# Performance work log

Measured on AMD Instinct MI355X. Metric: run time of the kernel, lower is better.

The kernel has to match this reference:

```python
import jax, jax.numpy as jnp
import numpy as np

# Static config matching AdaConv(c_in=512, p=4, batch_size=8, s_d=512, c_out=512)
C_IN = 512
C_OUT = 512
N_GROUPS = 128  # c_in // p


def _conv(x, w, b, groups=1, padding='VALID'):
    # x: NCHW, w: OIHW
    y = jax.lax.conv_general_dilated(
        x, w, window_strides=(1, 1), padding=padding,
        dimension_numbers=('NCHW', 'OIHW', 'NCHW'),
        feature_group_count=groups)
    return y + b[None, :, None, None]


def setup_inputs() -> dict:
    key = jax.random.key(0)
    ks = jax.random.split(key, 9)
    f32 = jnp.float32
    s = 0.02  # small init scale to keep activations well-behaved
    inp = {
        'style_encoding': jax.random.normal(ks[0], (8, 512, 4, 4), f32),
        'predicted': jax.random.normal(ks[1], (8, 512, 64, 64), f32),
        'dw1_w': jax.random.normal(ks[2], (512, 512, 1, 1), f32) * s,
        'dw1_b': jnp.full((512,), 0.01, f32),
        'dw2_w': jax.random.normal(ks[3], (2048, 512, 2, 2), f32) * s,
        'dw2_b': jnp.full((2048,), 0.01, f32),
        'pk1_w': jax.random.normal(ks[4], (512, 512, 1, 1), f32) * s,
        'pk1_b': jnp.full((512,), 0.01, f32),
        'pk2_w': jax.random.normal(ks[5], (2048, 512, 1, 1), f32) * s,
        'pk2_b': jnp.full((2048,), 0.01, f32),
        'pb1_w': jax.random.normal(ks[6], (512, 512, 1, 1), f32) * s,
        'pb1_b': jnp.full((512,), 0.01, f32),
        'pb2_w': jax.random.normal(ks[7], (512, 512, 1, 1), f32) * s,
        'pb2_b': jnp.full((512,), 0.01, f32),
    }
    return inp


def reference(style_encoding, predicted,
              dw1_w, dw1_b, dw2_w, dw2_b,
              pk1_w, pk1_b, pk2_w, pk2_b,
              pb1_w, pb1_b, pb2_w, pb2_b):
    N = style_encoding.shape[0]
    lrelu = lambda x: jax.nn.leaky_relu(x, 0.01)

    # --- predict per-sample depthwise 3x3 kernels from style (4x4 -> 3x3) ---
    h = lrelu(_conv(style_encoding, dw1_w, dw1_b))           # [N, c_in, 4, 4]
    depthwise = _conv(h, dw2_w, dw2_b)                       # [N, c_out*(c_in/n_groups), 3, 3]
    depthwise = depthwise.reshape(N * C_OUT, C_IN // N_GROUPS, 3, 3)

    # --- predict per-sample pointwise kernels + bias from pooled style ---
    s_pool = jnp.mean(style_encoding, axis=(2, 3), keepdims=True)  # [N, s_d, 1, 1]
    pk = _conv(lrelu(_conv(s_pool, pk1_w, pk1_b)), pk2_w, pk2_b)
    pointwise_kn = pk.reshape(N * C_OUT, C_OUT // N_GROUPS, 1, 1)
    pb = _conv(lrelu(_conv(s_pool, pb1_w, pb1_b)), pb2_w, pb2_b)
    pointwise_bias = pb.reshape(N * C_OUT)

    # --- apply per-sample dynamic conv via huge-group grouped conv trick ---
    a, b, c, d = predicted.shape
    x = predicted.reshape(1, a * b, c, d)
    x = jnp.pad(x, ((0, 0), (0, 0), (1, 1), (1, 1)), mode='reflect')
    batch_groups = N * N_GROUPS
    y = jax.lax.conv_general_dilated(
        x, depthwise, (1, 1), 'VALID',
        dimension_numbers=('NCHW', 'OIHW', 'NCHW'),
        feature_group_count=batch_groups)                    # [1, N*c_out, c, d]
    y = jax.lax.conv_general_dilated(
        y, pointwise_kn, (1, 1), 'VALID',
        dimension_numbers=('NCHW', 'OIHW', 'NCHW'),
        feature_group_count=batch_groups)
    y = y + pointwise_bias[None, :, None, None]
    # permute([1,0,2,3]).view(a,b,c,d) with leading dim 1 == plain reshape
    return y.reshape(a, b, c, d)
```

## Files before the change

### kernel.cpp

```cpp
#include <hip/hip_runtime.h>

#define LRELU(x) ((x) > 0.f ? (x) : 0.01f * (x))

#define H2_OFF    0
#define T1_OFF    65536
#define T2_OFF    69632
#define PK_OFF    73728
#define PB_OFF    90112
#define D_OFF     94208
#define WB_OFF    241664

__global__ __launch_bounds__(256) void kA(const float* __restrict__ style,
    const float* __restrict__ dw1_w, const float* __restrict__ dw1_b,
    const float* __restrict__ pk1_w, const float* __restrict__ pk1_b,
    const float* __restrict__ pb1_w, const float* __restrict__ pb1_b,
    float* __restrict__ h2, float* __restrict__ t1, float* __restrict__ t2,
    float* __restrict__ D) {
  int b = blockIdx.x;
  int tid = threadIdx.x;
  __shared__ float smem[512];
  if (b >= 576) {
    int idx = (b - 576) * 256 + tid;
    float4 z; z.x = 0.f; z.y = 0.f; z.z = 0.f; z.w = 0.f;
    for (int j = idx; j < 36864; j += 16384) ((float4*)D)[j] = z;
    return;
  }
  int wave = tid >> 6, l = tid & 63;
  float sv[8];
  const float* w;
  const float* bv;
  float* outp;
  int cobase;
  bool relu;
  if (b < 512) {
    int n = b >> 6; int pix = (b >> 2) & 15; int cq = b & 3;
    const float* sp = style + n * 8192 + pix;
#pragma unroll
    for (int j = 0; j < 8; ++j) sv[j] = sp[(8 * l + j) * 16];
    w = dw1_w; bv = dw1_b;
    cobase = cq * 128 + wave * 32;
    outp = h2 + n * 8192 + pix * 512;
    relu = true;
  } else {
    int b2 = b - 512;
    int cq = b2 & 3; int which = (b2 >> 2) & 1; int n = b2 >> 3;
    for (int ci = tid; ci < 512; ci += 256) {
      const float4* r4 = (const float4*)(style + n * 8192 + ci * 16);
      float4 a = r4[0], bb = r4[1], c = r4[2], d = r4[3];
      smem[ci] = (a.x+a.y+a.z+a.w + bb.x+bb.y+bb.z+bb.w + c.x+c.y+c.z+c.w + d.x+d.y+d.z+d.w) * (1.f/16.f);
    }
    __syncthreads();
#pragma unroll
    for (int j = 0; j < 8; ++j) sv[j] = smem[8 * l + j];
    w  = which ? pb1_w : pk1_w;
    bv = which ? pb1_b : pk1_b;
    cobase = cq * 128 + wave * 32;
    outp = (which ? t2 : t1) + n * 512;
    relu = true;
  }
  float res = (l < 32) ? bv[cobase + l] : 0.f;
#pragma unroll 8
  for (int j = 0; j < 32; ++j) {
    int co = cobase + j;
    const float4* wr = (const float4*)(w + co * 512 + 8 * l);
    float4 a = wr[0], c = wr[1];
    float v = a.x*sv[0] + a.y*sv[1] + a.z*sv[2] + a.w*sv[3]
            + c.x*sv[4] + c.y*sv[5] + c.z*sv[6] + c.w*sv[7];
    v += __shfl_xor(v, 1);
    v += __shfl_xor(v, 2);
    v += __shfl_xor(v, 4);
    v += __shfl_xor(v, 8);
    v += __shfl_xor(v, 16);
    v += __shfl_xor(v, 32);
    if (l == j) res += v;
  }
  if (l < 32) {
    float o = relu ? LRELU(res) : res;
    outp[cobase + l] = o;
  }
}

__global__ __launch_bounds__(256) void kB(const float* __restrict__ h2,
    const float* __restrict__ dw2_w,
    const float* __restrict__ t1, const float* __restrict__ t2,
    const float* __restrict__ pk2_w, const float* __restrict__ pk2_b,
    const float* __restrict__ pb2_w, const float* __restrict__ pb2_b,
    float* __restrict__ D, float* __restrict__ pk, float* __restrict__ pb) {
  __shared__ float smem[1280];
  int b = blockIdx.x;
  int tid = threadIdx.x;
  if (b < 512) {
    int kc = b & 31; int bt = b >> 5; int bo = bt & 7; int nh = bt >> 3;
    {
      int pix = tid & 15; int ci4 = (tid >> 4) & 3; int nn = tid >> 6;
      const float* src = h2 + (nh * 4 + nn) * 8192 + pix * 512 + kc * 16 + ci4 * 4;
      float4 v = *(const float4*)src;
      float* dst = &smem[(nn * 16 + ci4 * 4) * 20 + pix];
      dst[0]  = v.x;
      dst[20] = v.y;
      dst[40] = v.z;
      dst[60] = v.w;
    }
    __syncthreads();
    int o2 = bo * 256 + tid;
    const float4* wr = (const float4*)(dw2_w + o2 * 2048 + kc * 64);
    float acc[4][9];
#pragma unroll
    for (int nn = 0; nn < 4; ++nn)
#pragma unroll
      for (int p = 0; p < 9; ++p) acc[nn][p] = 0.f;
    for (int ci = 0; ci < 16; ++ci) {
      float4 wv = wr[ci];
#pragma unroll
      for (int nn = 0; nn < 4; ++nn) {
        const float* hrow = &smem[(nn * 16 + ci) * 20];
        float4 a0 = *(const float4*)(hrow + 0);
        float4 a1 = *(const float4*)(hrow + 4);
        float4 a2 = *(const float4*)(hrow + 8);
        float4 a3 = *(const float4*)(hrow + 12);
        float vv[16];
        vv[0]=a0.x; vv[1]=a0.y; vv[2]=a0.z; vv[3]=a0.w;
        vv[4]=a1.x; vv[5]=a1.y; vv[6]=a1.z; vv[7]=a1.w;
        vv[8]=a2.x; vv[9]=a2.y; vv[10]=a2.z; vv[11]=a2.w;
        vv[12]=a3.x; vv[13]=a3.y; vv[14]=a3.z; vv[15]=a3.w;
#pragma unroll
        for (int p = 0; p < 9; ++p) {
          int r = (p / 3) * 4 + (p % 3);
          acc[nn][p] += wv.x * vv[r] + wv.y * vv[r + 1] + wv.z * vv[r + 4] + wv.w * vv[r + 5];
        }
      }
    }
#pragma unroll
    for (int nn = 0; nn < 4; ++nn)
#pragma unroll
      for (int p = 0; p < 9; ++p)
        atomicAdd(&D[((nh * 4 + nn) * 9 + p) * 2048 + o2], acc[nn][p]);
  } else {
    int idx = b - 512;
    int n = idx / 10; int tile = idx % 10;
    bool isPb = tile >= 8;
    float* s = smem;
    const float* src = (isPb ? t2 : t1) + n * 512;
    for (int i = tid; i < 512; i += 256) s[i] = src[i];
    __syncthreads();
    int o = (isPb ? tile - 8 : tile) * 256 + tid;
    const float* w = isPb ? pb2_w : pk2_w;
    float acc = (isPb ? pb2_b : pk2_b)[o];
    const float4* wr = (const float4*)(w + o * 512);
#pragma unroll 8
    for (int k = 0; k < 128; ++k) {
      float4 wv = wr[k];
      acc += wv.x * s[4*k] + wv.y * s[4*k+1] + wv.z * s[4*k+2] + wv.w * s[4*k+3];
    }
    if (isPb) pb[n * 512 + o] = acc; else pk[n * 2048 + o] = acc;
  }
}

__global__ __launch_bounds__(256) void kW(const float* __restrict__ D,
    const float* __restrict__ pk, const float* __restrict__ dw2_b,
    const float* __restrict__ pb, float* __restrict__ wbuf) {
  int idx = blockIdx.x * 256 + threadIdx.x;
  if (idx >= 8 * 128 * 160) return;
  int t = idx % 160; int Qn = idx / 160; int Q = Qn & 127; int n = Qn >> 7;
  if (t >= 144) {
    wbuf[idx] = (t < 148) ? pb[n * 512 + Q * 4 + (t - 144)] : 0.f;
    return;
  }
  int o = t & 3; int u = t >> 2; int kx = u % 3; int v = u / 3;
  int i = v & 3; int ky = v >> 2; int p = ky * 3 + kx;
  const float* Dp  = D + (n * 9 + p) * 2048 + 16 * Q;
  const float* pkp = pk + n * 2048 + 16 * Q + 4 * o;
  const float* bp  = dw2_b + 16 * Q;
  float sum = 0.f;
#pragma unroll
  for (int j = 0; j < 4; ++j) sum += pkp[j] * (Dp[4 * j + i] + bp[4 * j + i]);
  wbuf[idx] = sum;
}

__global__ __launch_bounds__(256) void kC(const float* __restrict__ x,
    const float* __restrict__ wbuf, float* __restrict__ out) {
  int b = blockIdx.x; int rt = b & 3; int Q = (b >> 2) & 127; int n = b >> 9;
  const float* wb = wbuf + (size_t)(n * 128 + Q) * 160;
  const float* base = x + (size_t)(n * 512 + Q * 4) * 4096;
  int e = threadIdx.x & 15;
  int y = rt * 16 + (threadIdx.x >> 4);
  int x0 = 4 * e;
  int ro[3];
#pragma unroll
  for (int ky = 0; ky < 3; ++ky) {
    int ry = y - 1 + ky;
    ry = ry < 0 ? 1 : (ry > 63 ? 62 : ry);
    ro[ky] = ry * 64;
  }
  float acc[4][4];
#pragma unroll
  for (int o = 0; o < 4; ++o) {
    float bv = wb[144 + o];
#pragma unroll
    for (int px = 0; px < 4; ++px) acc[o][px] = bv;
  }
#pragma unroll
  for (int i = 0; i < 4; ++i) {
    const float* ci = base + i * 4096;
#pragma unroll
    for (int ky = 0; ky < 3; ++ky) {
      float4 v0 = *(const float4*)(ci + ro[ky] + x0);
      float vl = __shfl_up(v0.w, 1, 16);
      float vr = __shfl_down(v0.x, 1, 16);
      if (e == 0)  vl = v0.y;
      if (e == 15) vr = v0.z;
      float va0 = vl, va1 = v0.x, va2 = v0.y, va3 = v0.z, va4 = v0.w, va5 = vr;
#pragma unroll
      for (int kx = 0; kx < 3; ++kx) {
        const float* wp = &wb[((ky * 4 + i) * 3 + kx) * 4];
        float w0 = wp[0], w1 = wp[1], w2 = wp[2], w3 = wp[3];
        float xv0 = kx == 0 ? va0 : (kx == 1 ? va1 : va2);
        float xv1 = kx == 0 ? va1 : (kx == 1 ? va2 : va3);
        float xv2 = kx == 0 ? va2 : (kx == 1 ? va3 : va4);
        float xv3 = kx == 0 ? va3 : (kx == 1 ? va4 : va5);
        acc[0][0] += w0 * xv0; acc[0][1] += w0 * xv1; acc[0][2] += w0 * xv2; acc[0][3] += w0 * xv3;
        acc[1][0] += w1 * xv0; acc[1][1] += w1 * xv1; acc[1][2] += w1 * xv2; acc[1][3] += w1 * xv3;
        acc[2][0] += w2 * xv0; acc[2][1] += w2 * xv1; acc[2][2] += w2 * xv2; acc[2][3] += w2 * xv3;
        acc[3][0] += w3 * xv0; acc[3][1] += w3 * xv1; acc[3][2] += w3 * xv2; acc[3][3] += w3 * xv3;
      }
    }
  }
#pragma unroll
  for (int o = 0; o < 4; ++o) {
    float4 st; st.x = acc[o][0]; st.y = acc[o][1]; st.z = acc[o][2]; st.w = acc[o][3];
    *(float4*)&out[(((size_t)(n * 512 + Q * 4 + o)) * 64 + y) * 64 + x0] = st;
  }
}

extern "C" void kernel_launch(void* const* d_in, const int* in_sizes, int n_in,
                              void* d_out, int out_size, void* d_ws, size_t ws_size,
                              hipStream_t stream) {
  const float* style = (const float*)d_in[0];
  const float* pred  = (const float*)d_in[1];
  const float* dw1_w = (const float*)d_in[2];
  const float* dw1_b = (const float*)d_in[3];
  const float* dw2_w = (const float*)d_in[4];
  const float* dw2_b = (const float*)d_in[5];
  const float* pk1_w = (const float*)d_in[6];
  const float* pk1_b = (const float*)d_in[7];
  const float* pk2_w = (const float*)d_in[8];
  const float* pk2_b = (const float*)d_in[9];
  const float* pb1_w = (const float*)d_in[10];
  const float* pb1_b = (const float*)d_in[11];
  const float* pb2_w = (const float*)d_in[12];
  const float* pb2_b = (const float*)d_in[13];
  float* ws = (float*)d_ws;
  float* h2 = ws + H2_OFF;
  float* t1 = ws + T1_OFF;
  float* t2 = ws + T2_OFF;
  float* pk = ws + PK_OFF;
  float* pb = ws + PB_OFF;
  float* D  = ws + D_OFF;
  float* wb = ws + WB_OFF;
  float* out = (float*)d_out;

  kA<<<640, 256, 0, stream>>>(style, dw1_w, dw1_b, pk1_w, pk1_b, pb1_w, pb1_b, h2, t1, t2, D);
  kB<<<592, 256, 0, stream>>>(h2, dw2_w, t1, t2, pk2_w, pk2_b, pb2_w, pb2_b, D, pk, pb);
  kW<<<640, 256, 0, stream>>>(D, pk, dw2_b, pb, wb);
  kC<<<4096, 256, 0, stream>>>(pred, wb, out);
}
```

Measured before the change: 86.67 us.

## Stage dw2 weights through LDS with coalesced loads and split kB finer

The dw2 part of kB now loads its weight tile cooperatively into shared memory with coalesced float4 reads, replacing per-thread strided row reads. The input-channel chunk is halved, so there are twice as many blocks and twice as many atomicAdds into D. The pk2/pb2 matvec is rewritten to use the wave-wide shuffle-reduction pattern, which gives coalesced weight rows instead of one row per thread. LDS use rises to about 39KB per block, which may lower occupancy.

```diff
diff --git a/kernel.cpp b/kernel.cpp
--- a/kernel.cpp
+++ b/kernel.cpp
@@ -31,7 +31,6 @@
   const float* bv;
   float* outp;
   int cobase;
-  bool relu;
   if (b < 512) {
     int n = b >> 6; int pix = (b >> 2) & 15; int cq = b & 3;
     const float* sp = style + n * 8192 + pix;
@@ -40,7 +39,6 @@
     w = dw1_w; bv = dw1_b;
     cobase = cq * 128 + wave * 32;
     outp = h2 + n * 8192 + pix * 512;
-    relu = true;
   } else {
     int b2 = b - 512;
     int cq = b2 & 3; int which = (b2 >> 2) & 1; int n = b2 >> 3;
@@ -56,7 +54,6 @@
     bv = which ? pb1_b : pk1_b;
     cobase = cq * 128 + wave * 32;
     outp = (which ? t2 : t1) + n * 512;
-    relu = true;
   }
   float res = (l < 32) ? bv[cobase + l] : 0.f;
 #pragma unroll 8
@@ -74,10 +71,7 @@
     v += __shfl_xor(v, 32);
     if (l == j) res += v;
   }
-  if (l < 32) {
-    float o = relu ? LRELU(res) : res;
-    outp[cobase + l] = o;
-  }
+  if (l < 32) outp[cobase + l] = LRELU(res);
 }
 
 __global__ __launch_bounds__(256) void kB(const float* __restrict__ h2,
@@ -86,34 +80,43 @@
     const float* __restrict__ pk2_w, const float* __restrict__ pk2_b,
     const float* __restrict__ pb2_w, const float* __restrict__ pb2_b,
     float* __restrict__ D, float* __restrict__ pk, float* __restrict__ pb) {
-  __shared__ float smem[1280];
+  __shared__ float smem[9856];
   int b = blockIdx.x;
   int tid = threadIdx.x;
-  if (b < 512) {
-    int kc = b & 31; int bt = b >> 5; int bo = bt & 7; int nh = bt >> 3;
-    {
-      int pix = tid & 15; int ci4 = (tid >> 4) & 3; int nn = tid >> 6;
-      const float* src = h2 + (nh * 4 + nn) * 8192 + pix * 512 + kc * 16 + ci4 * 4;
+  if (b < 1024) {
+    int kc = b & 63; int bo = (b >> 6) & 7; int nh = b >> 9;
+    float* Wt = smem;
+    float* ht = smem + 9216;
+    if (tid < 128) {
+      int pix = tid & 15; int cq = (tid >> 4) & 1; int nn = tid >> 5;
+      const float* src = h2 + (nh * 4 + nn) * 8192 + pix * 512 + kc * 8 + cq * 4;
       float4 v = *(const float4*)src;
-      float* dst = &smem[(nn * 16 + ci4 * 4) * 20 + pix];
+      float* dst = &ht[(nn * 8 + cq * 4) * 20 + pix];
       dst[0]  = v.x;
       dst[20] = v.y;
       dst[40] = v.z;
       dst[60] = v.w;
     }
+#pragma unroll
+    for (int m = 0; m < 8; ++m) {
+      int fidx = m * 1024 + tid * 4;
+      int row = fidx >> 5; int col = fidx & 31;
+      float4 v = *(const float4*)(dw2_w + (size_t)(bo * 256 + row) * 2048 + kc * 32 + col);
+      *(float4*)&Wt[row * 36 + col] = v;
+    }
     __syncthreads();
     int o2 = bo * 256 + tid;
-    const float4* wr = (const float4*)(dw2_w + o2 * 2048 + kc * 64);
     float acc[4][9];
 #pragma unroll
     for (int nn = 0; nn < 4; ++nn)
 #pragma unroll
       for (int p = 0; p < 9; ++p) acc[nn][p] = 0.f;
-    for (int ci = 0; ci < 16; ++ci) {
-      float4 wv = wr[ci];
+#pragma unroll
+    for (int ci = 0; ci < 8; ++ci) {
+      float4 wv = *(const float4*)&Wt[tid * 36 + 4 * ci];
 #pragma unroll
       for (int nn = 0; nn < 4; ++nn) {
-        const float* hrow = &smem[(nn * 16 + ci) * 20];
+        const float* hrow = &ht[(nn * 8 + ci) * 20];
         float4 a0 = *(const float4*)(hrow + 0);
         float4 a1 = *(const float4*)(hrow + 4);
         float4 a2 = *(const float4*)(hrow + 8);
@@ -136,23 +139,41 @@
       for (int p = 0; p < 9; ++p)
         atomicAdd(&D[((nh * 4 + nn) * 9 + p) * 2048 + o2], acc[nn][p]);
   } else {
-    int idx = b - 512;
-    int n = idx / 10; int tile = idx % 10;
-    bool isPb = tile >= 8;
+    int b2 = b - 1024;
+    int n = b2 / 20; int t20 = b2 % 20;
+    bool isPb = t20 >= 16;
+    int cobase = (isPb ? (t20 - 16) : t20) * 128;
     float* s = smem;
     const float* src = (isPb ? t2 : t1) + n * 512;
     for (int i = tid; i < 512; i += 256) s[i] = src[i];
     __syncthreads();
-    int o = (isPb ? tile - 8 : tile) * 256 + tid;
-    const float* w = isPb ? pb2_w : pk2_w;
-    float acc = (isPb ? pb2_b : pk2_b)[o];
-    const float4* wr = (const float4*)(w + o * 512);
+    int wave = tid >> 6, l = tid & 63;
+    float sv[8];
+#pragma unroll
+    for (int j = 0; j < 8; ++j) sv[j] = s[8 * l + j];
+    const float* w  = isPb ? pb2_w : pk2_w;
+    const float* bv = isPb ? pb2_b : pk2_b;
+    int cg = cobase + wave * 32;
+    float res = (l < 32) ? bv[cg + l] : 0.f;
 #pragma unroll 8
-    for (int k = 0; k < 128; ++k) {
-      float4 wv = wr[k];
-      acc += wv.x * s[4*k] + wv.y * s[4*k+1] + wv.z * s[4*k+2] + wv.w * s[4*k+3];
-    }
-    if (isPb) pb[n * 512 + o] = acc; else pk[n * 2048 + o] = acc;
+    for (int j = 0; j < 32; ++j) {
+      int co = cg + j;
+      const float4* wr = (const float4*)(w + co * 512 + 8 * l);
+      float4 a = wr[0], c = wr[1];
+      float v = a.x*sv[0] + a.y*sv[1] + a.z*sv[2] + a.w*sv[3]
+              + c.x*sv[4] + c.y*sv[5] + c.z*sv[6] + c.w*sv[7];
+      v += __shfl_xor(v, 1);
+      v += __shfl_xor(v, 2);
+      v += __shfl_xor(v, 4);
+      v += __shfl_xor(v, 8);
+      v += __shfl_xor(v, 16);
+      v += __shfl_xor(v, 32);
+      if (l == j) res += v;
+    }
+    if (l < 32) {
+      if (isPb) pb[n * 512 + cg + l] = res;
+      else      pk[n * 2048 + cg + l] = res;
+    }
   }
 }
 
@@ -260,7 +281,7 @@
   float* out = (float*)d_out;
 
   kA<<<640, 256, 0, stream>>>(style, dw1_w, dw1_b, pk1_w, pk1_b, pb1_w, pb1_b, h2, t1, t2, D);
-  kB<<<592, 256, 0, stream>>>(h2, dw2_w, t1, t2, pk2_w, pk2_b, pb2_w, pb2_b, D, pk, pb);
+  kB<<<1184, 256, 0, stream>>>(h2, dw2_w, t1, t2, pk2_w, pk2_b, pb2_w, pb2_b, D, pk, pb);
   kW<<<640, 256, 0, stream>>>(D, pk, dw2_b, pb, wb);
   kC<<<4096, 256, 0, stream>>>(pred, wb, out);
 }
```

New measurement: 95.87 us. 10.6% more time.
